# Kernel tuning notes

Measured on AMD Instinct MI355X. Metric: run time of the kernel, lower is better.

The kernel has to match this reference:

```python
import jax, jax.numpy as jnp
import numpy as np

T = 0.07  # softmax temperature from __init__
N_QUEUES = 4


def _l2norm(x, axis):
    return x / jnp.maximum(jnp.linalg.norm(x, axis=axis, keepdims=True), 1e-12)


def setup_inputs() -> dict:
    key = jax.random.key(0)
    k1, k2, k3, k4, k5, k6 = jax.random.split(key, 6)
    N, D_in, dim, K = 512, 2048, 128, 65536
    im_q = jax.random.normal(k1, (N, D_in), dtype=jnp.float32)
    im_k = jax.random.normal(k2, (N, D_in), dtype=jnp.float32)
    W_q = jax.random.normal(k3, (D_in, dim), dtype=jnp.float32) * (1.0 / np.sqrt(D_in))
    W_k = jax.random.normal(k4, (D_in, dim), dtype=jnp.float32) * (1.0 / np.sqrt(D_in))
    queues = jax.random.normal(k5, (N_QUEUES, dim, K), dtype=jnp.float32)
    queues = _l2norm(queues, axis=1)  # normalize along feature dim, as in __init__
    label = jax.random.randint(k6, (N,), 0, 4, dtype=jnp.int32)
    return {"im_q": im_q, "im_k": im_k, "W_q": W_q, "W_k": W_k,
            "queues": queues, "label": label}


def reference(im_q, im_k, W_q, W_k, queues, label):
    # encoder_q / encoder_k abstracted as linear projections
    q = _l2norm(im_q @ W_q, axis=1)                      # [N, C]
    k = _l2norm(im_k @ W_k, axis=1)                      # [N, C] (no_grad in original)
    l_pos = jnp.einsum('nc,nc->n', q, k)[:, None]        # [N, 1]
    # per-sample queue routing: queue index = (label - 1) % 4
    route = jnp.mod(label - 1, N_QUEUES)                 # [N]
    onehot = jax.nn.one_hot(route, N_QUEUES, dtype=q.dtype)  # [N, G]
    # l_neg[n, k] = sum_c q[n, c] * queues[route[n], c, k], as grouped matmul
    l_neg = jnp.einsum('ngc,gck->nk', q[:, None, :] * onehot[:, :, None], queues)  # [N, K]
    logits = jnp.concatenate([l_pos, l_neg], axis=1) / T  # [N, 1+K]
    labels = jnp.zeros(logits.shape[0], dtype=jnp.int32)
    return logits, labels
```

## Files before the change

kernel.cpp:

```cpp
#include <hip/hip_runtime.h>

typedef short short8 __attribute__((ext_vector_type(8)));
typedef float floatx4 __attribute__((ext_vector_type(4)));

__device__ __forceinline__ unsigned short f2bf(float f) {
  unsigned u = __float_as_uint(f);
  u += 0x7FFFu + ((u >> 16) & 1u);
  return (unsigned short)(u >> 16);
}

__global__ __launch_bounds__(512, 4) void proj_partial(
    const float* __restrict__ im_q, const float* __restrict__ im_k,
    const float* __restrict__ Wq, const float* __restrict__ Wk,
    float* __restrict__ part, int* __restrict__ cnt) {
  __shared__ float imS[16 * 260];
  const int t = threadIdx.x;
  if (blockIdx.x == 0 && blockIdx.y == 0 && blockIdx.z == 0 && t < 4) cnt[t] = 0;
  const int which = blockIdx.z;
  const float* __restrict__ im = which ? im_k : im_q;
  const float* __restrict__ W  = which ? Wk : Wq;
  const int d0 = blockIdx.x * 256;
  const int row0 = blockIdx.y * 16;
#pragma unroll
  for (int p = 0; p < 2; ++p) {
    const int idx = t + p * 512;
    const int r = idx >> 6;
    const int dd = (idx & 63) * 4;
    *(float4*)(imS + r * 260 + dd) =
        *(const float4*)(im + (size_t)(row0 + r) * 2048 + d0 + dd);
  }
  __syncthreads();
  const int c4 = (t & 31) * 4;
  const int r  = t >> 5;
  float acc0 = 0.f, acc1 = 0.f, acc2 = 0.f, acc3 = 0.f;
  const float* __restrict__ Wp = W + (size_t)d0 * 128 + c4;
#pragma unroll 8
  for (int d = 0; d < 256; ++d) {
    const float4 w = *(const float4*)(Wp + (size_t)d * 128);
    const float a = imS[r * 260 + d];
    acc0 += a * w.x; acc1 += a * w.y; acc2 += a * w.z; acc3 += a * w.w;
  }
  *(float4*)(part + ((size_t)(which * 8 + blockIdx.x) * 512 + row0 + r) * 128 + c4) =
      make_float4(acc0, acc1, acc2, acc3);
}

__global__ __launch_bounds__(128) void finalize(
    const float* __restrict__ part, const int* __restrict__ label,
    unsigned short* __restrict__ qbf, int* __restrict__ cnt,
    int* __restrict__ rows, float* __restrict__ out) {
  const int n = blockIdx.x, c = threadIdx.x;
  float qraw = 0.f, kraw = 0.f;
#pragma unroll
  for (int ch = 0; ch < 8; ++ch) {
    qraw += part[((size_t)ch * 512 + n) * 128 + c];
    kraw += part[((size_t)(8 + ch) * 512 + n) * 128 + c];
  }
  float sq = qraw * qraw, sk = kraw * kraw, dt = qraw * kraw;
#pragma unroll
  for (int off = 32; off > 0; off >>= 1) {
    sq += __shfl_down(sq, off, 64);
    sk += __shfl_down(sk, off, 64);
    dt += __shfl_down(dt, off, 64);
  }
  __shared__ float sh[3][2];
  const int lane = c & 63, wv = c >> 6;
  if (lane == 0) { sh[0][wv] = sq; sh[1][wv] = sk; sh[2][wv] = dt; }
  __syncthreads();
  const float tsq = sh[0][0] + sh[0][1];
  const float tsk = sh[1][0] + sh[1][1];
  const float tdt = sh[2][0] + sh[2][1];
  const float nq = fmaxf(sqrtf(tsq), 1e-12f);
  const float nk = fmaxf(sqrtf(tsk), 1e-12f);
  qbf[n * 128 + c] = f2bf(qraw / nq);
  if (c == 0) {
    out[(size_t)n * 65537] = tdt / (nq * nk) * (1.0f / 0.07f);
    ((int*)out)[(size_t)512 * 65537 + n] = 0;
    int g = ((label[n] - 1) % 4 + 4) % 4;
    int pos = atomicAdd(cnt + g, 1);
    rows[g * 512 + pos] = n;
  }
}

__global__ __launch_bounds__(256) void qpack(
    const unsigned short* __restrict__ qbf, const int* __restrict__ cnt,
    const int* __restrict__ rows, unsigned short* __restrict__ Apack) {
  const int g = blockIdx.x >> 2, ch = blockIdx.x & 3;
  const int Mg = cnt[g];
  const int t = threadIdx.x;
#pragma unroll
  for (int w = 0; w < 8; ++w) {
    const int slot = w * 256 + t;
    const int kk = slot >> 9;
    const int rb = (slot >> 6) & 7;
    const int lane = slot & 63;
    const int l16 = lane & 15, qd = lane >> 4;
    const int m = ch * 128 + rb * 16 + l16;
    uint4 v = make_uint4(0u, 0u, 0u, 0u);
    if (m < Mg) {
      const int n = rows[g * 512 + m];
      v = *(const uint4*)(qbf + (size_t)n * 128 + kk * 32 + qd * 8);
    }
    *(uint4*)(Apack + ((size_t)blockIdx.x * 2048 + slot) * 8) = v;
  }
}

__global__ __launch_bounds__(256, 2) void moco_lneg(
    const float* __restrict__ queues, const unsigned short* __restrict__ Apack,
    const int* __restrict__ cnt, const int* __restrict__ rows,
    float* __restrict__ out) {
  __shared__ int rowsS[512];
  const int g = blockIdx.y;
  const int Mg = cnt[g];
  if (Mg == 0) return;
  const int t = threadIdx.x;
  for (int i = t; i < 512; i += 256) rowsS[i] = rows[g * 512 + i];
  __syncthreads();
  const int lane = t & 63, wave = t >> 6;
  const int qd = lane >> 4, l16 = lane & 15;
  const float invT = 1.0f / 0.07f;
  const int valid0 = min(Mg, 128);
  const unsigned short* __restrict__ Ab =
      Apack + (size_t)g * 4 * 16384 + (size_t)lane * 8;

  for (int jt = 0; jt < 2; ++jt) {
    const int j0 = (blockIdx.x * 2 + jt) * 128;
    short8 bf[4][2];
    {
      const float* __restrict__ qb =
          queues + ((size_t)(g * 128 + qd * 8)) * 65536 + j0 + l16;
#pragma unroll
      for (int kk = 0; kk < 4; ++kk) {
#pragma unroll
        for (int s = 0; s < 2; ++s) {
          const float* __restrict__ p =
              qb + (size_t)(kk * 32) * 65536 + (wave * 2 + s) * 16;
          float f[8];
#pragma unroll
          for (int e = 0; e < 8; ++e) f[e] = p[(size_t)e * 65536];
          unsigned* d = (unsigned*)&bf[kk][s];
#pragma unroll
          for (int i = 0; i < 4; ++i)
            d[i] = (unsigned)f2bf(f[2 * i]) | ((unsigned)f2bf(f[2 * i + 1]) << 16);
        }
      }
    }
    floatx4 acc[8][2];
#pragma unroll
    for (int rb = 0; rb < 8; ++rb) {
      floatx4 z = {0.f, 0.f, 0.f, 0.f};
      acc[rb][0] = z; acc[rb][1] = z;
    }
    __builtin_amdgcn_s_setprio(1);
#pragma unroll
    for (int rb = 0; rb < 8; ++rb) {
      if (rb * 16 < valid0) {
#pragma unroll
        for (int kk = 0; kk < 4; ++kk) {
          const short8 afrag = *(const short8*)(Ab + kk * 4096 + rb * 512);
          acc[rb][0] = __builtin_amdgcn_mfma_f32_16x16x32_bf16(afrag, bf[kk][0], acc[rb][0], 0, 0, 0);
          acc[rb][1] = __builtin_amdgcn_mfma_f32_16x16x32_bf16(afrag, bf[kk][1], acc[rb][1], 0, 0, 0);
        }
      }
    }
    __builtin_amdgcn_s_setprio(0);
#pragma unroll
    for (int rb = 0; rb < 8; ++rb) {
      if (rb * 16 < valid0) {
#pragma unroll
        for (int r = 0; r < 4; ++r) {
          const int ml = rb * 16 + qd * 4 + r;
          if (ml < valid0) {
            const size_t base = (size_t)rowsS[ml] * 65537 + 1 + j0;
            out[base + (wave * 2 + 0) * 16 + l16] = acc[rb][0][r] * invT;
            out[base + (wave * 2 + 1) * 16 + l16] = acc[rb][1][r] * invT;
          }
        }
      }
    }
    for (int mb = 8; mb * 16 < Mg; ++mb) {
      const int chh = mb >> 3, rbi = mb & 7;
      const unsigned short* __restrict__ At =
          Apack + ((size_t)(g * 4 + chh) * 2048 + (size_t)lane) * 8;
      floatx4 a0 = {0.f, 0.f, 0.f, 0.f}, a1 = {0.f, 0.f, 0.f, 0.f};
#pragma unroll
      for (int kk = 0; kk < 4; ++kk) {
        const short8 afrag = *(const short8*)(At + kk * 4096 + rbi * 512);
        a0 = __builtin_amdgcn_mfma_f32_16x16x32_bf16(afrag, bf[kk][0], a0, 0, 0, 0);
        a1 = __builtin_amdgcn_mfma_f32_16x16x32_bf16(afrag, bf[kk][1], a1, 0, 0, 0);
      }
#pragma unroll
      for (int r = 0; r < 4; ++r) {
        const int ml = mb * 16 + qd * 4 + r;
        if (ml < Mg) {
          const size_t base = (size_t)rowsS[ml] * 65537 + 1 + j0;
          out[base + (wave * 2 + 0) * 16 + l16] = a0[r] * invT;
          out[base + (wave * 2 + 1) * 16 + l16] = a1[r] * invT;
        }
      }
    }
  }
}

extern "C" void kernel_launch(void* const* d_in, const int* in_sizes, int n_in,
                              void* d_out, int out_size, void* d_ws, size_t ws_size,
                              hipStream_t stream) {
  const float* im_q   = (const float*)d_in[0];
  const float* im_k   = (const float*)d_in[1];
  const float* Wq     = (const float*)d_in[2];
  const float* Wk     = (const float*)d_in[3];
  const float* queues = (const float*)d_in[4];
  const int*   label  = (const int*)d_in[5];
  float* out = (float*)d_out;

  char* ws = (char*)d_ws;
  float* part = (float*)ws;
  unsigned short* qbf = (unsigned short*)(ws + (4u << 20));
  int* cnt  = (int*)(ws + (4u << 20) + (128u << 10));
  int* rows = cnt + 4;
  unsigned short* Apack = (unsigned short*)ws;

  proj_partial<<<dim3(8, 32, 2), 512, 0, stream>>>(im_q, im_k, Wq, Wk, part, cnt);
  finalize<<<512, 128, 0, stream>>>(part, label, qbf, cnt, rows, out);
  qpack<<<16, 256, 0, stream>>>(qbf, cnt, rows, Apack);
  moco_lneg<<<dim3(256, 4), 256, 0, stream>>>(queues, Apack, cnt, rows, out);
}
```

Before: 334.0 us.

## Double-buffer queue tiles into LDS via async global_load_lds in l_neg kernel

The l_neg kernel now streams queue tiles of 128x64 floats into a double-buffered, XOR-swizzled LDS area using direct global-to-LDS loads, prefetching the next tile while computing the current one. Previously each thread did strided scalar global loads straight into registers. Each block now covers 512 columns in 8 tiles, so the grid is halved. The intent is to hide the queue read latency and coalesce the loads, at the cost of 64KB of LDS per block, which lowers occupancy and adds barriers.

```diff
diff --git a/kernel.cpp b/kernel.cpp
--- a/kernel.cpp
+++ b/kernel.cpp
@@ -7,6 +7,12 @@
   unsigned u = __float_as_uint(f);
   u += 0x7FFFu + ((u >> 16) & 1u);
   return (unsigned short)(u >> 16);
+}
+
+__device__ __forceinline__ void gload_lds16(const float* g, float* l) {
+  __builtin_amdgcn_global_load_lds(
+      (const __attribute__((address_space(1))) void*)g,
+      (__attribute__((address_space(3))) void*)l, 16, 0, 0);
 }
 
 __global__ __launch_bounds__(512, 4) void proj_partial(
@@ -108,48 +114,71 @@
     const float* __restrict__ queues, const unsigned short* __restrict__ Apack,
     const int* __restrict__ cnt, const int* __restrict__ rows,
     float* __restrict__ out) {
+  __shared__ float bufs[2][128 * 64];
   __shared__ int rowsS[512];
   const int g = blockIdx.y;
   const int Mg = cnt[g];
   if (Mg == 0) return;
   const int t = threadIdx.x;
+  const int lane = t & 63, wave = t >> 6;
+  const int qd = lane >> 4, l16 = lane & 15;
   for (int i = t; i < 512; i += 256) rowsS[i] = rows[g * 512 + i];
   __syncthreads();
-  const int lane = t & 63, wave = t >> 6;
-  const int qd = lane >> 4, l16 = lane & 15;
+
+  const int j0b = blockIdx.x * 512;
+  const float* __restrict__ qg = queues + (size_t)g * 128 * 65536;
   const float invT = 1.0f / 0.07f;
   const int valid0 = min(Mg, 128);
   const unsigned short* __restrict__ Ab =
       Apack + (size_t)g * 4 * 16384 + (size_t)lane * 8;
 
-  for (int jt = 0; jt < 2; ++jt) {
-    const int j0 = (blockIdx.x * 2 + jt) * 128;
-    short8 bf[4][2];
-    {
-      const float* __restrict__ qb =
-          queues + ((size_t)(g * 128 + qd * 8)) * 65536 + j0 + l16;
-#pragma unroll
-      for (int kk = 0; kk < 4; ++kk) {
-#pragma unroll
-        for (int s = 0; s < 2; ++s) {
-          const float* __restrict__ p =
-              qb + (size_t)(kk * 32) * 65536 + (wave * 2 + s) * 16;
-          float f[8];
-#pragma unroll
-          for (int e = 0; e < 8; ++e) f[e] = p[(size_t)e * 65536];
-          unsigned* d = (unsigned*)&bf[kk][s];
-#pragma unroll
-          for (int i = 0; i < 4; ++i)
-            d[i] = (unsigned)f2bf(f[2 * i]) | ((unsigned)f2bf(f[2 * i + 1]) << 16);
-        }
-      }
-    }
-    floatx4 acc[8][2];
-#pragma unroll
-    for (int rb = 0; rb < 8; ++rb) {
-      floatx4 z = {0.f, 0.f, 0.f, 0.f};
-      acc[rb][0] = z; acc[rb][1] = z;
-    }
+#define STAGE(tt)                                                              \
+  {                                                                            \
+    const int _b = (tt) & 1;                                                   \
+    _Pragma("unroll")                                                          \
+    for (int i = 0; i < 8; ++i) {                                              \
+      const int c0 = wave * 32 + i * 4;                                        \
+      const int x = (c0 >> 2) & 15;                                            \
+      const float* gp = qg + (size_t)(c0 + (lane >> 4)) * 65536 + j0b +        \
+                        (tt) * 64 + (((lane & 15) ^ x) << 2);                  \
+      gload_lds16(gp, &bufs[_b][c0 * 64]);                                     \
+    }                                                                          \
+  }
+
+  STAGE(0);
+  for (int tt = 0; tt < 8; ++tt) {
+    if (tt < 7) {
+      STAGE(tt + 1);
+      asm volatile("s_waitcnt vmcnt(8)" ::: "memory");
+    } else {
+      asm volatile("s_waitcnt vmcnt(0)" ::: "memory");
+    }
+    __builtin_amdgcn_sched_barrier(0);
+    __builtin_amdgcn_s_barrier();
+    __builtin_amdgcn_sched_barrier(0);
+
+    const float* __restrict__ bp = &bufs[tt & 1][0];
+    short8 bfrag[4];
+#pragma unroll
+    for (int kk = 0; kk < 4; ++kk) {
+      const int cb = kk * 32 + qd * 8;
+      const int chunk = wave * 4 + (l16 >> 2);
+      const int o = l16 & 3;
+      float f[8];
+#pragma unroll
+      for (int e = 0; e < 8; ++e) {
+        const int c = cb + e;
+        const int x = (c >> 2) & 15;
+        f[e] = bp[c * 64 + ((chunk ^ x) << 2) + o];
+      }
+      unsigned* d = (unsigned*)&bfrag[kk];
+#pragma unroll
+      for (int i = 0; i < 4; ++i)
+        d[i] = (unsigned)f2bf(f[2 * i]) | ((unsigned)f2bf(f[2 * i + 1]) << 16);
+    }
+    floatx4 acc[8];
+#pragma unroll
+    for (int rb = 0; rb < 8; ++rb) { floatx4 z = {0.f,0.f,0.f,0.f}; acc[rb] = z; }
     __builtin_amdgcn_s_setprio(1);
 #pragma unroll
     for (int rb = 0; rb < 8; ++rb) {
@@ -157,23 +186,20 @@
 #pragma unroll
         for (int kk = 0; kk < 4; ++kk) {
           const short8 afrag = *(const short8*)(Ab + kk * 4096 + rb * 512);
-          acc[rb][0] = __builtin_amdgcn_mfma_f32_16x16x32_bf16(afrag, bf[kk][0], acc[rb][0], 0, 0, 0);
-          acc[rb][1] = __builtin_amdgcn_mfma_f32_16x16x32_bf16(afrag, bf[kk][1], acc[rb][1], 0, 0, 0);
+          acc[rb] = __builtin_amdgcn_mfma_f32_16x16x32_bf16(afrag, bfrag[kk], acc[rb], 0, 0, 0);
         }
       }
     }
     __builtin_amdgcn_s_setprio(0);
+    const int jcol = j0b + tt * 64 + wave * 16 + l16;
 #pragma unroll
     for (int rb = 0; rb < 8; ++rb) {
       if (rb * 16 < valid0) {
 #pragma unroll
         for (int r = 0; r < 4; ++r) {
           const int ml = rb * 16 + qd * 4 + r;
-          if (ml < valid0) {
-            const size_t base = (size_t)rowsS[ml] * 65537 + 1 + j0;
-            out[base + (wave * 2 + 0) * 16 + l16] = acc[rb][0][r] * invT;
-            out[base + (wave * 2 + 1) * 16 + l16] = acc[rb][1][r] * invT;
-          }
+          if (ml < valid0)
+            out[(size_t)rowsS[ml] * 65537 + 1 + jcol] = acc[rb][r] * invT;
         }
       }
     }
@@ -181,24 +207,23 @@
       const int chh = mb >> 3, rbi = mb & 7;
       const unsigned short* __restrict__ At =
           Apack + ((size_t)(g * 4 + chh) * 2048 + (size_t)lane) * 8;
-      floatx4 a0 = {0.f, 0.f, 0.f, 0.f}, a1 = {0.f, 0.f, 0.f, 0.f};
+      floatx4 a0 = {0.f, 0.f, 0.f, 0.f};
 #pragma unroll
       for (int kk = 0; kk < 4; ++kk) {
         const short8 afrag = *(const short8*)(At + kk * 4096 + rbi * 512);
-        a0 = __builtin_amdgcn_mfma_f32_16x16x32_bf16(afrag, bf[kk][0], a0, 0, 0, 0);
-        a1 = __builtin_amdgcn_mfma_f32_16x16x32_bf16(afrag, bf[kk][1], a1, 0, 0, 0);
+        a0 = __builtin_amdgcn_mfma_f32_16x16x32_bf16(afrag, bfrag[kk], a0, 0, 0, 0);
       }
 #pragma unroll
       for (int r = 0; r < 4; ++r) {
         const int ml = mb * 16 + qd * 4 + r;
-        if (ml < Mg) {
-          const size_t base = (size_t)rowsS[ml] * 65537 + 1 + j0;
-          out[base + (wave * 2 + 0) * 16 + l16] = a0[r] * invT;
-          out[base + (wave * 2 + 1) * 16 + l16] = a1[r] * invT;
-        }
-      }
-    }
-  }
+        if (ml < Mg)
+          out[(size_t)rowsS[ml] * 65537 + 1 + jcol] = a0[r] * invT;
+      }
+    }
+    __builtin_amdgcn_s_barrier();
+    __builtin_amdgcn_sched_barrier(0);
+  }
+#undef STAGE
 }
 
 extern "C" void kernel_launch(void* const* d_in, const int* in_sizes, int n_in,
@@ -222,5 +247,5 @@
   proj_partial<<<dim3(8, 32, 2), 512, 0, stream>>>(im_q, im_k, Wq, Wk, part, cnt);
   finalize<<<512, 128, 0, stream>>>(part, label, qbf, cnt, rows, out);
   qpack<<<16, 256, 0, stream>>>(qbf, cnt, rows, Apack);
-  moco_lneg<<<dim3(256, 4), 256, 0, stream>>>(queues, Apack, cnt, rows, out);
-}
+  moco_lneg<<<dim3(128, 4), 256, 0, stream>>>(queues, Apack, cnt, rows, out);
+}
```

Result: slower. 352.8 us (+5.6%).
